# Kernel optimization log

Hardware: AMD Instinct MI355X
Metric: run time of the kernel (lower is better)

## Reference

```python
import jax, jax.numpy as jnp
import numpy as np

H = 4  # head_num = 8 // 2
NEG = -1e9


def mha(x, mask, wqkv, bqkv, wo, bo):
    # x: [B, N, D], mask: [B, 1, N] (0 = masked key), wqkv: [3, D, D], wo: [D, Dout]
    B, N, D = x.shape
    dh = D // H
    q = (x @ wqkv[0] + bqkv[0]).reshape(B, N, H, dh)
    k = (x @ wqkv[1] + bqkv[1]).reshape(B, N, H, dh)
    v = (x @ wqkv[2] + bqkv[2]).reshape(B, N, H, dh)
    scores = jnp.einsum('bqhd,bkhd->bhqk', q, k) / jnp.sqrt(jnp.asarray(dh, x.dtype))
    scores = jnp.where(mask[:, None, :, :] == 0, NEG, scores)  # mask keys, bcast over heads/queries
    attn = jax.nn.softmax(scores, axis=-1)
    out = jnp.einsum('bhqk,bkhd->bqhd', attn, v).reshape(B, N, D)
    return out @ wo + bo


def setup_inputs() -> dict:
    key = jax.random.key(0)
    ks = jax.random.split(key, 24)
    B, M, F = 16, 32, 16
    N = M * M
    def w(k, shape, fan_in):
        return jax.random.normal(k, shape, dtype=jnp.float32) / np.sqrt(fan_in)
    return {
        'robot_1_node': jax.random.normal(ks[0], (B, M, F), dtype=jnp.float32),
        'robot_2_node': jax.random.normal(ks[1], (B, M, F), dtype=jnp.float32),
        'coop_edge_cost': jax.random.normal(ks[2], (B, M, M, F), dtype=jnp.float32),
        'coop_edge_mask': jax.random.randint(ks[3], (B, M, M), 0, 2, dtype=jnp.int32),
        'd1_wqkv': w(ks[4], (3, 48, 48), 48), 'd1_bqkv': jnp.zeros((3, 48), jnp.float32),
        'd1_wo': w(ks[5], (48, 16), 48), 'd1_bo': jnp.zeros((16,), jnp.float32),
        'd2_wqkv': w(ks[6], (3, 16, 16), 16), 'd2_bqkv': jnp.zeros((3, 16), jnp.float32),
        'd2_wo': w(ks[7], (16, 16), 16), 'd2_bo': jnp.zeros((16,), jnp.float32),
        'pol_wqkv': w(ks[8], (3, 16, 16), 16), 'pol_bqkv': jnp.zeros((3, 16), jnp.float32),
        'pol_wo': w(ks[9], (16, 1), 16), 'pol_bo': jnp.zeros((1,), jnp.float32),
        'val_wqkv': w(ks[10], (3, 16, 16), 16), 'val_bqkv': jnp.zeros((3, 16), jnp.float32),
        'val_wo': w(ks[11], (16, 1), 16), 'val_bo': jnp.zeros((1,), jnp.float32),
        'v2_w': w(ks[12], (N, 16), N), 'v2_b': jnp.zeros((16,), jnp.float32),
    }


def reference(robot_1_node, robot_2_node, coop_edge_cost, coop_edge_mask,
              d1_wqkv, d1_bqkv, d1_wo, d1_bo,
              d2_wqkv, d2_bqkv, d2_wo, d2_bo,
              pol_wqkv, pol_bqkv, pol_wo, pol_bo,
              val_wqkv, val_bqkv, val_wo, val_bo,
              v2_w, v2_b):
    B, M, F = robot_1_node.shape
    N = M * M
    edge = coop_edge_cost.reshape(B, N, -1)            # flatten(-3,-2)
    mask = coop_edge_mask.reshape(B, 1, N)             # flatten + unsqueeze(-2)
    f1 = jnp.broadcast_to(robot_1_node[:, :, None, :], (B, M, M, F)).reshape(B, N, F)
    f2 = jnp.broadcast_to(robot_2_node[:, None, :, :], (B, M, M, F)).reshape(B, N, F)
    f = jnp.concatenate([f1, f2, edge], axis=-1)       # [B, N, 3F]
    e = mha(f, mask, d1_wqkv, d1_bqkv, d1_wo, d1_bo)   # [B, N, 16]
    e = mha(e, mask, d2_wqkv, d2_bqkv, d2_wo, d2_bo)   # [B, N, 16]
    action = mha(e, mask, pol_wqkv, pol_bqkv, pol_wo, pol_bo).reshape(B, N)
    masked_action = jax.nn.softmax(jnp.where(mask[:, 0, :] == 0, NEG, action), axis=-1)
    critic = mha(e, mask, val_wqkv, val_bqkv, val_wo, val_bo).reshape(B, N)
    critic = critic @ v2_w + v2_b                       # [B, 16]
    return masked_action, critic
```

## Files before the change

kernel.cpp:

```cpp
#include <hip/hip_runtime.h>
#include <math.h>

#define NEGV (-1e9f)
#define LOG2E 1.4426950408889634f

typedef _Float16 f16;
typedef __attribute__((ext_vector_type(2))) __fp16 hf2;
typedef __attribute__((ext_vector_type(4))) _Float16 f16x4;
typedef __attribute__((ext_vector_type(4))) float f32x4;

__global__ void qkv1_prep_kernel(
    const float* __restrict__ r1, const float* __restrict__ r2,
    const float* __restrict__ edge,
    const float* __restrict__ d1_wqkv, const float* __restrict__ d1_bqkv,
    const float* __restrict__ d1_wo, const float* __restrict__ d1_bo,
    const float* __restrict__ d2_wqkv, const float* __restrict__ d2_bqkv,
    const float* __restrict__ d2_wo, const float* __restrict__ d2_bo,
    const float* __restrict__ pol_wqkv, const float* __restrict__ pol_bqkv,
    const float* __restrict__ val_wqkv, const float* __restrict__ val_bqkv,
    f16* __restrict__ q1h, f16* __restrict__ k1h, f16* __restrict__ v1h,
    float* __restrict__ Wf1, float* __restrict__ bf1,
    float* __restrict__ Wfp, float* __restrict__ bfp,
    float* __restrict__ Wfv, float* __restrict__ bfv,
    int B, int M, int F, int H, float qmul1, int mainBlocks) {
    const int N = M * M;
    const int BN = B * N;

    if ((int)blockIdx.x < mainBlocks) {
        int t = blockIdx.x * blockDim.x + threadIdx.x;
        if (t >= 3 * BN * 48) return;
        int col = t % 48;
        int row = (t / 48) % BN;
        int mat = t / (48 * BN);
        int b = row / N, n = row % N;
        int i = n / M, j = n % M;

        const float* f1 = r1 + (b * M + i) * F;
        const float* f2 = r2 + (b * M + j) * F;
        const float* fe = edge + (size_t)row * F;
        const float* w  = d1_wqkv + mat * 48 * 48 + col;

        float s = d1_bqkv[mat * 48 + col];
#pragma unroll
        for (int d = 0; d < 16; ++d) s = fmaf(f1[d], w[d * 48], s);
#pragma unroll
        for (int d = 0; d < 16; ++d) s = fmaf(f2[d], w[(16 + d) * 48], s);
#pragma unroll
        for (int d = 0; d < 16; ++d) s = fmaf(fe[d], w[(32 + d) * 48], s);

        int h = col / 12, dd = col % 12;
        size_t off = ((size_t)(b * H + h) * N + n) * 12 + dd;
        if (mat == 0)      q1h[off] = (f16)(s * qmul1);
        else if (mat == 1) k1h[off] = (f16)s;
        else               v1h[off] = (f16)s;
        return;
    }

    int t = (blockIdx.x - mainBlocks) * blockDim.x + threadIdx.x;
    if (t < 2304) {
        int mat = t / 768, r = (t % 768) / 16, c = t % 16;
        float s = 0.f;
#pragma unroll
        for (int k = 0; k < 16; ++k)
            s = fmaf(d1_wo[r * 16 + k], d2_wqkv[mat * 256 + k * 16 + c], s);
        Wf1[t] = s;
        return;
    }
    int u = t - 2304;
    if (u < 48) {
        int mat = u / 16, c = u % 16;
        float s = d2_bqkv[mat * 16 + c];
#pragma unroll
        for (int k = 0; k < 16; ++k)
            s = fmaf(d1_bo[k], d2_wqkv[mat * 256 + k * 16 + c], s);
        bf1[u] = s;
        return;
    }
    u -= 48;
    if (u < 768) {
        int mat = u / 256, r = (u % 256) / 16, c = u % 16;
        float s = 0.f;
#pragma unroll
        for (int k = 0; k < 16; ++k)
            s = fmaf(d2_wo[r * 16 + k], pol_wqkv[mat * 256 + k * 16 + c], s);
        Wfp[u] = s;
        return;
    }
    u -= 768;
    if (u < 48) {
        int mat = u / 16, c = u % 16;
        float s = pol_bqkv[mat * 16 + c];
#pragma unroll
        for (int k = 0; k < 16; ++k)
            s = fmaf(d2_bo[k], pol_wqkv[mat * 256 + k * 16 + c], s);
        bfp[u] = s;
        return;
    }
    u -= 48;
    if (u < 768) {
        int mat = u / 256, r = (u % 256) / 16, c = u % 16;
        float s = 0.f;
#pragma unroll
        for (int k = 0; k < 16; ++k)
            s = fmaf(d2_wo[r * 16 + k], val_wqkv[mat * 256 + k * 16 + c], s);
        Wfv[u] = s;
        return;
    }
    u -= 768;
    if (u < 48) {
        int mat = u / 16, c = u % 16;
        float s = val_bqkv[mat * 16 + c];
#pragma unroll
        for (int k = 0; k < 16; ++k)
            s = fmaf(d2_bo[k], val_wqkv[mat * 256 + k * 16 + c], s);
        bfv[u] = s;
    }
}

template <int DH, int QT>
__global__ __launch_bounds__(256, 8) void attn_h_kernel(
    const f16* __restrict__ qh1, const f16* __restrict__ kh1, const f16* __restrict__ vh1,
    const f16* __restrict__ qh2, const f16* __restrict__ kh2, const f16* __restrict__ vh2,
    const int* __restrict__ mask,
    float* __restrict__ pacc1, float* __restrict__ pl1,
    float* __restrict__ pacc2, float* __restrict__ pl2,
    int B, int H, int N) {
    const int LD = H * DH;
    const int BH = B * H;

    int bhs = blockIdx.x;
    const f16* qh; const f16* kh; const f16* vh;
    float* pacc; float* pl;
    if (bhs < BH) { qh = qh1; kh = kh1; vh = vh1; pacc = pacc1; pl = pl1; }
    else          { qh = qh2; kh = kh2; vh = vh2; pacc = pacc2; pl = pl2; bhs -= BH; }
    int b = bhs / H, h = bhs % H;
    int kbase = blockIdx.z * 256;
    int bN = b * N;

    __shared__ __align__(16) f16 Kt[256][DH];
    __shared__ __align__(16) f16 Vt[16][264];
    __shared__ __align__(16) float mbs[256];

    int tid = threadIdx.x;
    {
        int kk = tid;
        const f16* kB = kh + ((size_t)bhs * N + kbase) * DH;
        const f16* vB = vh + ((size_t)bhs * N + kbase) * DH;
#pragma unroll
        for (int d = 0; d < DH / 4; ++d)
            ((uint2*)&Kt[kk][0])[d] = ((const uint2*)(kB + (size_t)kk * DH))[d];
        uint2 vr[DH / 4];
#pragma unroll
        for (int d = 0; d < DH / 4; ++d)
            vr[d] = ((const uint2*)(vB + (size_t)kk * DH))[d];
        const f16* vv = (const f16*)vr;
#pragma unroll
        for (int d = 0; d < DH; ++d) Vt[d][kk] = vv[d];
        Vt[DH][kk] = (f16)1.f;
        mbs[kk] = mask[bN + kbase + kk] ? (-8.f * LOG2E) : NEGV;
    }
    __syncthreads();

    int lane = tid & 63, wid = tid >> 6;
    int lrow = lane & 15, lg = lane >> 4;
    int qbase = blockIdx.y * (QT * 64) + wid * (QT * 16);

    const f16* qB = qh + (size_t)bhs * N * DH;
    f16x4 zf = {(f16)0.f, (f16)0.f, (f16)0.f, (f16)0.f};
    bool qok = (4 * lg < DH);
    f16x4 qf[QT];
#pragma unroll
    for (int qt = 0; qt < QT; ++qt)
        qf[qt] = qok ? *(const f16x4*)(qB + (size_t)(qbase + qt * 16 + lrow) * DH + 4 * lg) : zf;

    f32x4 oacc[QT];
#pragma unroll
    for (int qt = 0; qt < QT; ++qt) oacc[qt] = (f32x4){0.f, 0.f, 0.f, 0.f};

#pragma unroll 8
    for (int t16 = 0; t16 < 16; ++t16) {
        f16x4 kf = *(const f16x4*)(&Kt[0][0] + (size_t)(t16 * 16 + lrow) * DH + 4 * lg);
        float4 mv = *(const float4*)(&mbs[t16 * 16 + 4 * lg]);
        f32x4 mc = {mv.x, mv.y, mv.z, mv.w};
        f16x4 vb = *(const f16x4*)(&Vt[lrow][t16 * 16 + 4 * lg]);

#pragma unroll
        for (int qt = 0; qt < QT; ++qt) {
            f32x4 s = __builtin_amdgcn_mfma_f32_16x16x16f16(kf, qf[qt], mc, 0, 0, 0);
            hf2 lo = __builtin_amdgcn_cvt_pkrtz(__builtin_amdgcn_exp2f(s[0]),
                                                __builtin_amdgcn_exp2f(s[1]));
            hf2 hi = __builtin_amdgcn_cvt_pkrtz(__builtin_amdgcn_exp2f(s[2]),
                                                __builtin_amdgcn_exp2f(s[3]));
            f16x4 pa;
            ((hf2*)&pa)[0] = lo;
            ((hf2*)&pa)[1] = hi;
            oacc[qt] = __builtin_amdgcn_mfma_f32_16x16x16f16(pa, vb, oacc[qt], 0, 0, 0);
        }
    }

    int d = lrow;
    size_t zoff = (size_t)blockIdx.z * B * N;
#pragma unroll
    for (int qt = 0; qt < QT; ++qt) {
#pragma unroll
        for (int r = 0; r < 4; ++r) {
            int q = qbase + qt * 16 + lg * 4 + r;
            float val = oacc[qt][r];
            if (d < DH)
                pacc[(zoff + bN + q) * LD + h * DH + d] = val;
            else if (d == DH)
                pl[(zoff + bN + q) * H + h] = val;
        }
    }
}

__global__ __launch_bounds__(256) void fold1_kernel(
    const float* __restrict__ pacc, const float* __restrict__ pl,
    const float* __restrict__ Wf1, const float* __restrict__ bf1,
    f16* __restrict__ q2h, f16* __restrict__ k2h, f16* __restrict__ v2h,
    int BN, int N, int H, float qmul2) {
    int row0 = blockIdx.x * 16;
    int tid = threadIdx.x;
    __shared__ float comb[16][49];
    __shared__ float invl[16][4];
    if (tid < 64) {
        int r = tid >> 2, h = tid & 3;
        float ls = 0.f;
#pragma unroll
        for (int z = 0; z < 4; ++z) ls += pl[((size_t)z * BN + row0 + r) * 4 + h];
        invl[r][h] = 1.f / ls;
    }
    __syncthreads();
#pragma unroll
    for (int k = 0; k < 3; ++k) {
        int idx = tid + k * 256;
        int r = idx / 48, d = idx % 48;
        float a = 0.f;
#pragma unroll
        for (int z = 0; z < 4; ++z) a += pacc[((size_t)z * BN + row0 + r) * 48 + d];
        comb[r][d] = a * invl[r][d / 12];
    }
    __syncthreads();
#pragma unroll
    for (int k = 0; k < 3; ++k) {
        int idx = tid + k * 256;
        int mat = idx / 256, r = (idx % 256) / 16, c = idx % 16;
        float s = bf1[mat * 16 + c];
        const float* wcol = Wf1 + mat * 768 + c;
#pragma unroll
        for (int d = 0; d < 48; ++d)
            s = fmaf(comb[r][d], wcol[d * 16], s);
        int row = row0 + r;
        int b = row / N, n = row % N;
        int h = c >> 2, dd = c & 3;
        size_t off = ((size_t)(b * H + h) * N + n) * 4 + dd;
        if (mat == 0)      q2h[off] = (f16)(s * qmul2);
        else if (mat == 1) k2h[off] = (f16)s;
        else               v2h[off] = (f16)s;
    }
}

__global__ __launch_bounds__(256) void fold2_kernel(
    const float* __restrict__ pacc, const float* __restrict__ pl,
    const float* __restrict__ Wfp, const float* __restrict__ bfp,
    const float* __restrict__ Wfv, const float* __restrict__ bfv,
    f16* __restrict__ qph, f16* __restrict__ kph, f16* __restrict__ vph,
    f16* __restrict__ qvh, f16* __restrict__ kvh, f16* __restrict__ vvh,
    int BN, int N, int H, float qmul2) {
    int row0 = blockIdx.x * 8;
    int tid = threadIdx.x;
    __shared__ float comb[8][17];
    __shared__ float invl[8][4];
    if (tid < 32) {
        int r = tid >> 2, h = tid & 3;
        float ls = 0.f;
#pragma unroll
        for (int z = 0; z < 4; ++z) ls += pl[((size_t)z * BN + row0 + r) * 4 + h];
        invl[r][h] = 1.f / ls;
    }
    __syncthreads();
    if (tid < 128) {
        int r = tid / 16, d = tid % 16;
        float a = 0.f;
#pragma unroll
        for (int z = 0; z < 4; ++z) a += pacc[((size_t)z * BN + row0 + r) * 16 + d];
        comb[r][d] = a * invl[r][d >> 2];
    }
    __syncthreads();
#pragma unroll
    for (int k = 0; k < 3; ++k) {
        int idx = tid + k * 256;
        int set = idx / 384;
        int rem = idx % 384;
        int mat = rem / 128, r = (rem % 128) / 16, c = rem % 16;
        const float* W  = set ? Wfv : Wfp;
        const float* bb = set ? bfv : bfp;
        float s = bb[mat * 16 + c];
        const float* wcol = W + mat * 256 + c;
#pragma unroll
        for (int d = 0; d < 16; ++d)
            s = fmaf(comb[r][d], wcol[d * 16], s);
        int row = row0 + r;
        int b = row / N, n = row % N;
        int h = c >> 2, dd = c & 3;
        size_t off = ((size_t)(b * H + h) * N + n) * 4 + dd;
        f16* dst;
        if (set == 0) dst = (mat == 0) ? qph : (mat == 1) ? kph : vph;
        else          dst = (mat == 0) ? qvh : (mat == 1) ? kvh : vvh;
        dst[off] = (f16)((mat == 0) ? s * qmul2 : s);
    }
}

__global__ __launch_bounds__(256) void final2_kernel(
    const float* __restrict__ paccp, const float* __restrict__ plp,
    const float* __restrict__ paccv, const float* __restrict__ plv,
    const float* __restrict__ pol_wo, const float* __restrict__ pol_bo,
    const float* __restrict__ val_wo, const float* __restrict__ val_bo,
    const int* __restrict__ mask, const float* __restrict__ v2w,
    const float* __restrict__ v2b,
    float* __restrict__ out_action, float* __restrict__ out_critic,
    int N, int B, int BN) {
    int tid = threadIdx.x;
    if ((int)blockIdx.x < B) {
        int b = blockIdx.x;
        int lane = tid & 63, wid = tid >> 6;
        __shared__ float wred[4];
        __shared__ float sbcast;

        float local[4];
        float mx = -INFINITY;
#pragma unroll
        for (int i = 0; i < 4; ++i) {
            int row = b * N + tid + i * 256;
            float sa = pol_bo[0];
            float ls0 = 0.f, ls1 = 0.f, ls2 = 0.f, ls3 = 0.f;
#pragma unroll
            for (int z = 0; z < 4; ++z) {
                const float* plr = plp + ((size_t)z * BN + row) * 4;
                ls0 += plr[0]; ls1 += plr[1]; ls2 += plr[2]; ls3 += plr[3];
            }
            float inv[4] = {1.f / ls0, 1.f / ls1, 1.f / ls2, 1.f / ls3};
#pragma unroll
            for (int d = 0; d < 16; ++d) {
                float a = 0.f;
#pragma unroll
                for (int z = 0; z < 4; ++z)
                    a += paccp[((size_t)z * BN + row) * 16 + d];
                sa = fmaf(a * inv[d >> 2], pol_wo[d], sa);
            }
            float aa = (mask[row] == 0) ? NEGV : sa;
            local[i] = aa;
            mx = fmaxf(mx, aa);
        }
#pragma unroll
        for (int o = 32; o > 0; o >>= 1) mx = fmaxf(mx, __shfl_down(mx, o));
        if (lane == 0) wred[wid] = mx;
        __syncthreads();
        if (tid == 0) sbcast = fmaxf(fmaxf(wred[0], wred[1]), fmaxf(wred[2], wred[3]));
        __syncthreads();
        mx = sbcast;

        float s = 0.f;
#pragma unroll
        for (int i = 0; i < 4; ++i) {
            float p = __expf(local[i] - mx);
            local[i] = p;
            s += p;
        }
#pragma unroll
        for (int o = 32; o > 0; o >>= 1) s += __shfl_down(s, o);
        if (lane == 0) wred[wid] = s;
        __syncthreads();
        if (tid == 0) sbcast = wred[0] + wred[1] + wred[2] + wred[3];
        __syncthreads();
        float inv = 1.f / sbcast;
#pragma unroll
        for (int i = 0; i < 4; ++i) out_action[b * N + tid + i * 256] = local[i] * inv;
    } else {
        int b = blockIdx.x - B;
        __shared__ float cr[1024];
        __shared__ float red[16][17];
#pragma unroll
        for (int i = 0; i < 4; ++i) {
            int idx = tid + i * 256;
            int row = b * N + idx;
            float sc = val_bo[0];
            float ls0 = 0.f, ls1 = 0.f, ls2 = 0.f, ls3 = 0.f;
#pragma unroll
            for (int z = 0; z < 4; ++z) {
                const float* plr = plv + ((size_t)z * BN + row) * 4;
                ls0 += plr[0]; ls1 += plr[1]; ls2 += plr[2]; ls3 += plr[3];
            }
            float inv[4] = {1.f / ls0, 1.f / ls1, 1.f / ls2, 1.f / ls3};
#pragma unroll
            for (int d = 0; d < 16; ++d) {
                float a = 0.f;
#pragma unroll
                for (int z = 0; z < 4; ++z)
                    a += paccv[((size_t)z * BN + row) * 16 + d];
                sc = fmaf(a * inv[d >> 2], val_wo[d], sc);
            }
            cr[idx] = sc;
        }
        __syncthreads();
        int c = tid & 15, seg = tid >> 4;
        float s = 0.f;
        int n0 = seg * 64;
        for (int n = n0; n < n0 + 64; ++n)
            s = fmaf(cr[n], v2w[n * 16 + c], s);
        red[seg][c] = s;
        __syncthreads();
        if (tid < 16) {
            float acc = v2b[tid];
#pragma unroll
            for (int g = 0; g < 16; ++g) acc += red[g][tid];
            out_critic[b * 16 + tid] = acc;
        }
    }
}

extern "C" void kernel_launch(void* const* d_in, const int* in_sizes, int n_in,
                              void* d_out, int out_size, void* d_ws, size_t ws_size,
                              hipStream_t stream) {
    const int B = 16, M = 32, F = 16, H = 4;
    const int N = M * M;
    const int BN = B * N;
    const int BHN = B * H * N;
    const int KSPLIT = 4;

    const float* r1       = (const float*)d_in[0];
    const float* r2       = (const float*)d_in[1];
    const float* edge     = (const float*)d_in[2];
    const int*   mask     = (const int*)d_in[3];
    const float* d1_wqkv  = (const float*)d_in[4];
    const float* d1_bqkv  = (const float*)d_in[5];
    const float* d1_wo    = (const float*)d_in[6];
    const float* d1_bo    = (const float*)d_in[7];
    const float* d2_wqkv  = (const float*)d_in[8];
    const float* d2_bqkv  = (const float*)d_in[9];
    const float* d2_wo    = (const float*)d_in[10];
    const float* d2_bo    = (const float*)d_in[11];
    const float* pol_wqkv = (const float*)d_in[12];
    const float* pol_bqkv = (const float*)d_in[13];
    const float* pol_wo   = (const float*)d_in[14];
    const float* pol_bo   = (const float*)d_in[15];
    const float* val_wqkv = (const float*)d_in[16];
    const float* val_bqkv = (const float*)d_in[17];
    const float* val_wo   = (const float*)d_in[18];
    const float* val_bo   = (const float*)d_in[19];
    const float* v2_w     = (const float*)d_in[20];
    const float* v2_b     = (const float*)d_in[21];

    float* ws = (float*)d_ws;
    float* pacc = ws;
    float* plp  = pacc + 4 * BN * 48;
    float* plv  = plp + 4 * BN * 4;
    float* Wf1  = plv + 4 * BN * 4;
    float* bf1  = Wf1 + 2304;
    float* Wfp  = bf1 + 48;
    float* bfp  = Wfp + 768;
    float* Wfv  = bfp + 48;
    float* bfv  = Wfv + 768;
    f16* fh  = (f16*)(bfv + 48);
    f16* q1h = fh;
    f16* k1h = q1h + (size_t)BHN * 12;
    f16* v1h = k1h + (size_t)BHN * 12;
    f16* q2h = v1h + (size_t)BHN * 12;
    f16* k2h = q2h + (size_t)BHN * 4;
    f16* v2h = k2h + (size_t)BHN * 4;
    f16* qph = v2h + (size_t)BHN * 4;
    f16* kph = qph + (size_t)BHN * 4;
    f16* vph = kph + (size_t)BHN * 4;
    f16* qvh = vph + (size_t)BHN * 4;
    f16* kvh = qvh + (size_t)BHN * 4;
    f16* vvh = kvh + (size_t)BHN * 4;
    float* paccp = pacc;
    float* paccv = pacc + (size_t)KSPLIT * BN * 16;

    float* out_action = (float*)d_out;
    float* out_critic = out_action + BN;

    const float qmul1 = (1.0f / sqrtf(12.0f)) * LOG2E;
    const float qmul2 = 0.5f * LOG2E;

    {
        int mainBlocks = (3 * BN * 48 + 255) / 256;
        qkv1_prep_kernel<<<mainBlocks + 16, 256, 0, stream>>>(
            r1, r2, edge, d1_wqkv, d1_bqkv, d1_wo, d1_bo,
            d2_wqkv, d2_bqkv, d2_wo, d2_bo,
            pol_wqkv, pol_bqkv, val_wqkv, val_bqkv,
            q1h, k1h, v1h, Wf1, bf1, Wfp, bfp, Wfv, bfv,
            B, M, F, H, qmul1, mainBlocks);
    }
    attn_h_kernel<12, 2><<<dim3(B * H, N / 128, KSPLIT), 256, 0, stream>>>(
        q1h, k1h, v1h, q1h, k1h, v1h, mask,
        pacc, plp, pacc, plp, B, H, N);
    fold1_kernel<<<BN / 16, 256, 0, stream>>>(
        pacc, plp, Wf1, bf1, q2h, k2h, v2h, BN, N, H, qmul2);
    attn_h_kernel<4, 2><<<dim3(B * H, N / 128, KSPLIT), 256, 0, stream>>>(
        q2h, k2h, v2h, q2h, k2h, v2h, mask,
        pacc, plp, pacc, plp, B, H, N);
    fold2_kernel<<<BN / 8, 256, 0, stream>>>(
        pacc, plp, Wfp, bfp, Wfv, bfv,
        qph, kph, vph, qvh, kvh, vvh, BN, N, H, qmul2);
    attn_h_kernel<4, 2><<<dim3(2 * B * H, N / 128, KSPLIT), 256, 0, stream>>>(
        qph, kph, vph, qvh, kvh, vvh, mask,
        paccp, plp, paccv, plv, B, H, N);
    final2_kernel<<<2 * B, 256, 0, stream>>>(
        paccp, plp, paccv, plv, pol_wo, pol_bo, val_wo, val_bo,
        mask, v2_w, v2_b, out_action, out_critic, N, B, BN);
}
```

Baseline: 105.0 us.

## Fuse attention with fold projections and drop split-K partial buffers

Each attention layer is restructured so one 512-thread block handles 32 queries across all 4 heads of one batch. It loops over all 1024 keys in four shared-memory chunks instead of splitting keys over grid z and writing partial accumulators. The normalized per-head output stays in shared memory and goes straight into the next layer's QKV projection (or the pol/val output head), which removes the separate fold kernels and the partial-sum global round trips. The cost is less grid parallelism, a longer serial key loop per block, and extra barriers per chunk.

```diff
diff --git a/kernel.cpp b/kernel.cpp
--- a/kernel.cpp
+++ b/kernel.cpp
@@ -56,7 +56,7 @@
         return;
     }
 
-    int t = (blockIdx.x - mainBlocks) * blockDim.x + threadIdx.x;
+    int t = (blockIdx.x - mainBlocks) * 256 + threadIdx.x;
     if (t < 2304) {
         int mat = t / 768, r = (t % 768) / 16, c = t % 16;
         float s = 0.f;
@@ -117,76 +117,58 @@
     }
 }
 
-template <int DH, int QT>
-__global__ __launch_bounds__(256, 8) void attn_h_kernel(
-    const f16* __restrict__ qh1, const f16* __restrict__ kh1, const f16* __restrict__ vh1,
-    const f16* __restrict__ qh2, const f16* __restrict__ kh2, const f16* __restrict__ vh2,
-    const int* __restrict__ mask,
-    float* __restrict__ pacc1, float* __restrict__ pl1,
-    float* __restrict__ pacc2, float* __restrict__ pl2,
-    int B, int H, int N) {
-    const int LD = H * DH;
-    const int BH = B * H;
-
-    int bhs = blockIdx.x;
-    const f16* qh; const f16* kh; const f16* vh;
-    float* pacc; float* pl;
-    if (bhs < BH) { qh = qh1; kh = kh1; vh = vh1; pacc = pacc1; pl = pl1; }
-    else          { qh = qh2; kh = kh2; vh = vh2; pacc = pacc2; pl = pl2; bhs -= BH; }
-    int b = bhs / H, h = bhs % H;
-    int kbase = blockIdx.z * 256;
-    int bN = b * N;
-
-    __shared__ __align__(16) f16 Kt[256][DH];
-    __shared__ __align__(16) f16 Vt[16][264];
-    __shared__ __align__(16) float mbs[256];
-
+template <int DH>
+__device__ inline void attn_core(const f16* __restrict__ qh, const f16* __restrict__ kh,
+                                 const f16* __restrict__ vh, const int* __restrict__ mask,
+                                 int b, int qg, int H, int N,
+                                 f16* __restrict__ Kt, f16* __restrict__ Vt,
+                                 float* __restrict__ mbs,
+                                 float* __restrict__ comb, int combStride) {
     int tid = threadIdx.x;
-    {
-        int kk = tid;
-        const f16* kB = kh + ((size_t)bhs * N + kbase) * DH;
-        const f16* vB = vh + ((size_t)bhs * N + kbase) * DH;
-#pragma unroll
-        for (int d = 0; d < DH / 4; ++d)
-            ((uint2*)&Kt[kk][0])[d] = ((const uint2*)(kB + (size_t)kk * DH))[d];
-        uint2 vr[DH / 4];
-#pragma unroll
-        for (int d = 0; d < DH / 4; ++d)
-            vr[d] = ((const uint2*)(vB + (size_t)kk * DH))[d];
-        const f16* vv = (const f16*)vr;
-#pragma unroll
-        for (int d = 0; d < DH; ++d) Vt[d][kk] = vv[d];
-        Vt[DH][kk] = (f16)1.f;
-        mbs[kk] = mask[bN + kbase + kk] ? (-8.f * LOG2E) : NEGV;
-    }
-    __syncthreads();
-
-    int lane = tid & 63, wid = tid >> 6;
+    int wave = tid >> 6, lane = tid & 63;
+    int h = wave & 3, qhalf = wave >> 2;
     int lrow = lane & 15, lg = lane >> 4;
-    int qbase = blockIdx.y * (QT * 64) + wid * (QT * 16);
-
-    const f16* qB = qh + (size_t)bhs * N * DH;
+    int bhs = b * H + h;
+    int qrow = qg * 32 + qhalf * 16 + lrow;
+
     f16x4 zf = {(f16)0.f, (f16)0.f, (f16)0.f, (f16)0.f};
     bool qok = (4 * lg < DH);
-    f16x4 qf[QT];
-#pragma unroll
-    for (int qt = 0; qt < QT; ++qt)
-        qf[qt] = qok ? *(const f16x4*)(qB + (size_t)(qbase + qt * 16 + lrow) * DH + 4 * lg) : zf;
-
-    f32x4 oacc[QT];
-#pragma unroll
-    for (int qt = 0; qt < QT; ++qt) oacc[qt] = (f32x4){0.f, 0.f, 0.f, 0.f};
-
+    f16x4 qf = qok ? *(const f16x4*)(qh + ((size_t)bhs * N + qrow) * DH + 4 * lg) : zf;
+
+    f32x4 oacc = {0.f, 0.f, 0.f, 0.f};
+
+    for (int chunk = 0; chunk < 4; ++chunk) {
+        int kbase = chunk * 256;
+        __syncthreads();
+        for (int idx = tid; idx < 1024; idx += 512) {
+            int hh = idx >> 8, kk = idx & 255;
+            const f16* kB = kh + ((size_t)(b * H + hh) * N + kbase + kk) * DH;
+            const f16* vB = vh + ((size_t)(b * H + hh) * N + kbase + kk) * DH;
+#pragma unroll
+            for (int d4 = 0; d4 < DH / 4; ++d4)
+                ((uint2*)(Kt + ((size_t)hh * 256 + kk) * DH))[d4] = ((const uint2*)kB)[d4];
+            uint2 vr[DH / 4];
+#pragma unroll
+            for (int d4 = 0; d4 < DH / 4; ++d4) vr[d4] = ((const uint2*)vB)[d4];
+            const f16* vv = (const f16*)vr;
+#pragma unroll
+            for (int d = 0; d < DH; ++d)
+                Vt[(hh * (DH + 1) + d) * 264 + kk] = vv[d];
+            Vt[(hh * (DH + 1) + DH) * 264 + kk] = (f16)1.f;
+        }
+        if (tid < 256) mbs[tid] = mask[b * N + kbase + tid] ? (-8.f * LOG2E) : NEGV;
+        __syncthreads();
+
+        const f16* KtH = Kt + (size_t)h * 256 * DH;
+        const f16* VtH = Vt + (size_t)h * (DH + 1) * 264;
 #pragma unroll 8
-    for (int t16 = 0; t16 < 16; ++t16) {
-        f16x4 kf = *(const f16x4*)(&Kt[0][0] + (size_t)(t16 * 16 + lrow) * DH + 4 * lg);
-        float4 mv = *(const float4*)(&mbs[t16 * 16 + 4 * lg]);
-        f32x4 mc = {mv.x, mv.y, mv.z, mv.w};
-        f16x4 vb = *(const f16x4*)(&Vt[lrow][t16 * 16 + 4 * lg]);
-
-#pragma unroll
-        for (int qt = 0; qt < QT; ++qt) {
-            f32x4 s = __builtin_amdgcn_mfma_f32_16x16x16f16(kf, qf[qt], mc, 0, 0, 0);
+        for (int t16 = 0; t16 < 16; ++t16) {
+            f16x4 kf = *(const f16x4*)(KtH + (size_t)(t16 * 16 + lrow) * DH + 4 * lg);
+            float4 mv = *(const float4*)(mbs + t16 * 16 + 4 * lg);
+            f32x4 mc = {mv.x, mv.y, mv.z, mv.w};
+            f16x4 vb = *(const f16x4*)(VtH + (size_t)lrow * 264 + t16 * 16 + 4 * lg);
+
+            f32x4 s = __builtin_amdgcn_mfma_f32_16x16x16f16(kf, qf, mc, 0, 0, 0);
             hf2 lo = __builtin_amdgcn_cvt_pkrtz(__builtin_amdgcn_exp2f(s[0]),
                                                 __builtin_amdgcn_exp2f(s[1]));
             hf2 hi = __builtin_amdgcn_cvt_pkrtz(__builtin_amdgcn_exp2f(s[2]),
@@ -194,116 +176,90 @@
             f16x4 pa;
             ((hf2*)&pa)[0] = lo;
             ((hf2*)&pa)[1] = hi;
-            oacc[qt] = __builtin_amdgcn_mfma_f32_16x16x16f16(pa, vb, oacc[qt], 0, 0, 0);
+            oacc = __builtin_amdgcn_mfma_f32_16x16x16f16(pa, vb, oacc, 0, 0, 0);
         }
     }
 
-    int d = lrow;
-    size_t zoff = (size_t)blockIdx.z * B * N;
-#pragma unroll
-    for (int qt = 0; qt < QT; ++qt) {
-#pragma unroll
-        for (int r = 0; r < 4; ++r) {
-            int q = qbase + qt * 16 + lg * 4 + r;
-            float val = oacc[qt][r];
-            if (d < DH)
-                pacc[(zoff + bN + q) * LD + h * DH + d] = val;
-            else if (d == DH)
-                pl[(zoff + bN + q) * H + h] = val;
-        }
-    }
-}
-
-__global__ __launch_bounds__(256) void fold1_kernel(
-    const float* __restrict__ pacc, const float* __restrict__ pl,
+    __syncthreads();
+#pragma unroll
+    for (int r = 0; r < 4; ++r) {
+        float lr = __shfl(oacc[r], (lane & 48) | DH);
+        if (lrow < DH)
+            comb[(qhalf * 16 + lg * 4 + r) * combStride + h * DH + lrow] = oacc[r] / lr;
+    }
+    __syncthreads();
+}
+
+__global__ __launch_bounds__(512, 4) void attn1_fold1_kernel(
+    const f16* __restrict__ q1h, const f16* __restrict__ k1h, const f16* __restrict__ v1h,
+    const int* __restrict__ mask,
     const float* __restrict__ Wf1, const float* __restrict__ bf1,
     f16* __restrict__ q2h, f16* __restrict__ k2h, f16* __restrict__ v2h,
-    int BN, int N, int H, float qmul2) {
-    int row0 = blockIdx.x * 16;
+    int H, int N, float qmul2) {
+    const int DH = 12;
+    const int VROWS = 3 * (DH + 1) + 16;
+    __shared__ __align__(16) f16 KtA[4 * 256 * DH];
+    __shared__ __align__(16) f16 VtA[VROWS * 264];
+    __shared__ __align__(16) float mbsA[256];
+
+    int qg = blockIdx.x, b = blockIdx.y;
+    float* comb = (float*)KtA;
+    attn_core<DH>(q1h, k1h, v1h, mask, b, qg, H, N, KtA, VtA, mbsA, comb, 49);
+
     int tid = threadIdx.x;
-    __shared__ float comb[16][49];
-    __shared__ float invl[16][4];
-    if (tid < 64) {
-        int r = tid >> 2, h = tid & 3;
-        float ls = 0.f;
-#pragma unroll
-        for (int z = 0; z < 4; ++z) ls += pl[((size_t)z * BN + row0 + r) * 4 + h];
-        invl[r][h] = 1.f / ls;
-    }
-    __syncthreads();
 #pragma unroll
     for (int k = 0; k < 3; ++k) {
-        int idx = tid + k * 256;
-        int r = idx / 48, d = idx % 48;
-        float a = 0.f;
-#pragma unroll
-        for (int z = 0; z < 4; ++z) a += pacc[((size_t)z * BN + row0 + r) * 48 + d];
-        comb[r][d] = a * invl[r][d / 12];
-    }
-    __syncthreads();
-#pragma unroll
-    for (int k = 0; k < 3; ++k) {
-        int idx = tid + k * 256;
-        int mat = idx / 256, r = (idx % 256) / 16, c = idx % 16;
+        int idx = tid + k * 512;
+        int mat = idx / 512, r = (idx % 512) / 16, c = idx % 16;
         float s = bf1[mat * 16 + c];
         const float* wcol = Wf1 + mat * 768 + c;
 #pragma unroll
         for (int d = 0; d < 48; ++d)
-            s = fmaf(comb[r][d], wcol[d * 16], s);
-        int row = row0 + r;
-        int b = row / N, n = row % N;
-        int h = c >> 2, dd = c & 3;
-        size_t off = ((size_t)(b * H + h) * N + n) * 4 + dd;
+            s = fmaf(comb[r * 49 + d], wcol[d * 16], s);
+        int n = qg * 32 + r;
+        int hh = c >> 2, dd = c & 3;
+        size_t off = ((size_t)(b * H + hh) * N + n) * 4 + dd;
         if (mat == 0)      q2h[off] = (f16)(s * qmul2);
         else if (mat == 1) k2h[off] = (f16)s;
         else               v2h[off] = (f16)s;
     }
 }
 
-__global__ __launch_bounds__(256) void fold2_kernel(
-    const float* __restrict__ pacc, const float* __restrict__ pl,
+__global__ __launch_bounds__(512, 8) void attn2_fold2_kernel(
+    const f16* __restrict__ q2h, const f16* __restrict__ k2h, const f16* __restrict__ v2h,
+    const int* __restrict__ mask,
     const float* __restrict__ Wfp, const float* __restrict__ bfp,
     const float* __restrict__ Wfv, const float* __restrict__ bfv,
     f16* __restrict__ qph, f16* __restrict__ kph, f16* __restrict__ vph,
     f16* __restrict__ qvh, f16* __restrict__ kvh, f16* __restrict__ vvh,
-    int BN, int N, int H, float qmul2) {
-    int row0 = blockIdx.x * 8;
+    int H, int N, float qmul2) {
+    const int DH = 4;
+    const int VROWS = 3 * (DH + 1) + 16;
+    __shared__ __align__(16) f16 KtA[4 * 256 * DH];
+    __shared__ __align__(16) f16 VtA[VROWS * 264];
+    __shared__ __align__(16) float mbsA[256];
+
+    int qg = blockIdx.x, b = blockIdx.y;
+    float* comb = (float*)KtA;
+    attn_core<DH>(q2h, k2h, v2h, mask, b, qg, H, N, KtA, VtA, mbsA, comb, 17);
+
     int tid = threadIdx.x;
-    __shared__ float comb[8][17];
-    __shared__ float invl[8][4];
-    if (tid < 32) {
-        int r = tid >> 2, h = tid & 3;
-        float ls = 0.f;
-#pragma unroll
-        for (int z = 0; z < 4; ++z) ls += pl[((size_t)z * BN + row0 + r) * 4 + h];
-        invl[r][h] = 1.f / ls;
-    }
-    __syncthreads();
-    if (tid < 128) {
-        int r = tid / 16, d = tid % 16;
-        float a = 0.f;
-#pragma unroll
-        for (int z = 0; z < 4; ++z) a += pacc[((size_t)z * BN + row0 + r) * 16 + d];
-        comb[r][d] = a * invl[r][d >> 2];
-    }
-    __syncthreads();
-#pragma unroll
-    for (int k = 0; k < 3; ++k) {
-        int idx = tid + k * 256;
-        int set = idx / 384;
-        int rem = idx % 384;
-        int mat = rem / 128, r = (rem % 128) / 16, c = rem % 16;
+#pragma unroll
+    for (int k = 0; k < 6; ++k) {
+        int idx = tid + k * 512;
+        int set = idx / 1536;
+        int rem = idx % 1536;
+        int mat = rem / 512, r = (rem % 512) / 16, c = rem % 16;
         const float* W  = set ? Wfv : Wfp;
         const float* bb = set ? bfv : bfp;
         float s = bb[mat * 16 + c];
         const float* wcol = W + mat * 256 + c;
 #pragma unroll
         for (int d = 0; d < 16; ++d)
-            s = fmaf(comb[r][d], wcol[d * 16], s);
-        int row = row0 + r;
-        int b = row / N, n = row % N;
-        int h = c >> 2, dd = c & 3;
-        size_t off = ((size_t)(b * H + h) * N + n) * 4 + dd;
+            s = fmaf(comb[r * 17 + d], wcol[d * 16], s);
+        int n = qg * 32 + r;
+        int hh = c >> 2, dd = c & 3;
+        size_t off = ((size_t)(b * H + hh) * N + n) * 4 + dd;
         f16* dst;
         if (set == 0) dst = (mat == 0) ? qph : (mat == 1) ? kph : vph;
         else          dst = (mat == 0) ? qvh : (mat == 1) ? kvh : vvh;
@@ -311,15 +267,43 @@
     }
 }
 
-__global__ __launch_bounds__(256) void final2_kernel(
-    const float* __restrict__ paccp, const float* __restrict__ plp,
-    const float* __restrict__ paccv, const float* __restrict__ plv,
+__global__ __launch_bounds__(512, 8) void attn3_heads_kernel(
+    const f16* __restrict__ qph, const f16* __restrict__ kph, const f16* __restrict__ vph,
+    const f16* __restrict__ qvh, const f16* __restrict__ kvh, const f16* __restrict__ vvh,
+    const int* __restrict__ mask,
     const float* __restrict__ pol_wo, const float* __restrict__ pol_bo,
     const float* __restrict__ val_wo, const float* __restrict__ val_bo,
-    const int* __restrict__ mask, const float* __restrict__ v2w,
+    float* __restrict__ araw, float* __restrict__ craw,
+    int H, int N) {
+    const int DH = 4;
+    const int VROWS = 3 * (DH + 1) + 16;
+    __shared__ __align__(16) f16 KtA[4 * 256 * DH];
+    __shared__ __align__(16) f16 VtA[VROWS * 264];
+    __shared__ __align__(16) float mbsA[256];
+
+    int qg = blockIdx.x, b = blockIdx.y, set = blockIdx.z;
+    const f16* qh = set ? qvh : qph;
+    const f16* kh = set ? kvh : kph;
+    const f16* vh = set ? vvh : vph;
+    float* comb = (float*)KtA;
+    attn_core<DH>(qh, kh, vh, mask, b, qg, H, N, KtA, VtA, mbsA, comb, 17);
+
+    int tid = threadIdx.x;
+    if (tid < 32) {
+        int r = tid;
+        const float* wo = set ? val_wo : pol_wo;
+        float s = (set ? val_bo : pol_bo)[0];
+#pragma unroll
+        for (int d = 0; d < 16; ++d) s = fmaf(comb[r * 17 + d], wo[d], s);
+        (set ? craw : araw)[b * N + qg * 32 + r] = s;
+    }
+}
+
+__global__ __launch_bounds__(256) void final_kernel(
+    const float* __restrict__ araw, const int* __restrict__ mask,
+    const float* __restrict__ craw, const float* __restrict__ v2w,
     const float* __restrict__ v2b,
-    float* __restrict__ out_action, float* __restrict__ out_critic,
-    int N, int B, int BN) {
+    float* __restrict__ out_action, float* __restrict__ out_critic, int N, int B) {
     int tid = threadIdx.x;
     if ((int)blockIdx.x < B) {
         int b = blockIdx.x;
@@ -331,26 +315,11 @@
         float mx = -INFINITY;
 #pragma unroll
         for (int i = 0; i < 4; ++i) {
-            int row = b * N + tid + i * 256;
-            float sa = pol_bo[0];
-            float ls0 = 0.f, ls1 = 0.f, ls2 = 0.f, ls3 = 0.f;
-#pragma unroll
-            for (int z = 0; z < 4; ++z) {
-                const float* plr = plp + ((size_t)z * BN + row) * 4;
-                ls0 += plr[0]; ls1 += plr[1]; ls2 += plr[2]; ls3 += plr[3];
-            }
-            float inv[4] = {1.f / ls0, 1.f / ls1, 1.f / ls2, 1.f / ls3};
-#pragma unroll
-            for (int d = 0; d < 16; ++d) {
-                float a = 0.f;
-#pragma unroll
-                for (int z = 0; z < 4; ++z)
-                    a += paccp[((size_t)z * BN + row) * 16 + d];
-                sa = fmaf(a * inv[d >> 2], pol_wo[d], sa);
-            }
-            float aa = (mask[row] == 0) ? NEGV : sa;
-            local[i] = aa;
-            mx = fmaxf(mx, aa);
+            int n = tid + i * 256;
+            float a = araw[b * N + n];
+            if (mask[b * N + n] == 0) a = NEGV;
+            local[i] = a;
+            mx = fmaxf(mx, a);
         }
 #pragma unroll
         for (int o = 32; o > 0; o >>= 1) mx = fmaxf(mx, __shfl_down(mx, o));
@@ -378,36 +347,12 @@
         for (int i = 0; i < 4; ++i) out_action[b * N + tid + i * 256] = local[i] * inv;
     } else {
         int b = blockIdx.x - B;
-        __shared__ float cr[1024];
+        int c = tid & 15, seg = tid >> 4;
         __shared__ float red[16][17];
-#pragma unroll
-        for (int i = 0; i < 4; ++i) {
-            int idx = tid + i * 256;
-            int row = b * N + idx;
-            float sc = val_bo[0];
-            float ls0 = 0.f, ls1 = 0.f, ls2 = 0.f, ls3 = 0.f;
-#pragma unroll
-            for (int z = 0; z < 4; ++z) {
-                const float* plr = plv + ((size_t)z * BN + row) * 4;
-                ls0 += plr[0]; ls1 += plr[1]; ls2 += plr[2]; ls3 += plr[3];
-            }
-            float inv[4] = {1.f / ls0, 1.f / ls1, 1.f / ls2, 1.f / ls3};
-#pragma unroll
-            for (int d = 0; d < 16; ++d) {
-                float a = 0.f;
-#pragma unroll
-                for (int z = 0; z < 4; ++z)
-                    a += paccv[((size_t)z * BN + row) * 16 + d];
-                sc = fmaf(a * inv[d >> 2], val_wo[d], sc);
-            }
-            cr[idx] = sc;
-        }
-        __syncthreads();
-        int c = tid & 15, seg = tid >> 4;
         float s = 0.f;
         int n0 = seg * 64;
         for (int n = n0; n < n0 + 64; ++n)
-            s = fmaf(cr[n], v2w[n * 16 + c], s);
+            s = fmaf(craw[b * N + n], v2w[n * 16 + c], s);
         red[seg][c] = s;
         __syncthreads();
         if (tid < 16) {
@@ -426,7 +371,6 @@
     const int N = M * M;
     const int BN = B * N;
     const int BHN = B * H * N;
-    const int KSPLIT = 4;
 
     const float* r1       = (const float*)d_in[0];
     const float* r2       = (const float*)d_in[1];
@@ -452,16 +396,15 @@
     const float* v2_b     = (const float*)d_in[21];
 
     float* ws = (float*)d_ws;
-    float* pacc = ws;
-    float* plp  = pacc + 4 * BN * 48;
-    float* plv  = plp + 4 * BN * 4;
-    float* Wf1  = plv + 4 * BN * 4;
+    float* Wf1  = ws;
     float* bf1  = Wf1 + 2304;
     float* Wfp  = bf1 + 48;
     float* bfp  = Wfp + 768;
     float* Wfv  = bfp + 48;
     float* bfv  = Wfv + 768;
-    f16* fh  = (f16*)(bfv + 48);
+    float* araw = bfv + 48;
+    float* craw = araw + BN;
+    f16* fh  = (f16*)(craw + BN);
     f16* q1h = fh;
     f16* k1h = q1h + (size_t)BHN * 12;
     f16* v1h = k1h + (size_t)BHN * 12;
@@ -474,8 +417,6 @@
     f16* qvh = vph + (size_t)BHN * 4;
     f16* kvh = qvh + (size_t)BHN * 4;
     f16* vvh = kvh + (size_t)BHN * 4;
-    float* paccp = pacc;
-    float* paccv = pacc + (size_t)KSPLIT * BN * 16;
 
     float* out_action = (float*)d_out;
     float* out_critic = out_action + BN;
@@ -492,21 +433,14 @@
             q1h, k1h, v1h, Wf1, bf1, Wfp, bfp, Wfv, bfv,
             B, M, F, H, qmul1, mainBlocks);
     }
-    attn_h_kernel<12, 2><<<dim3(B * H, N / 128, KSPLIT), 256, 0, stream>>>(
-        q1h, k1h, v1h, q1h, k1h, v1h, mask,
-        pacc, plp, pacc, plp, B, H, N);
-    fold1_kernel<<<BN / 16, 256, 0, stream>>>(
-        pacc, plp, Wf1, bf1, q2h, k2h, v2h, BN, N, H, qmul2);
-    attn_h_kernel<4, 2><<<dim3(B * H, N / 128, KSPLIT), 256, 0, stream>>>(
-        q2h, k2h, v2h, q2h, k2h, v2h, mask,
-        pacc, plp, pacc, plp, B, H, N);
-    fold2_kernel<<<BN / 8, 256, 0, stream>>>(
-        pacc, plp, Wfp, bfp, Wfv, bfv,
-        qph, kph, vph, qvh, kvh, vvh, BN, N, H, qmul2);
-    attn_h_kernel<4, 2><<<dim3(2 * B * H, N / 128, KSPLIT), 256, 0, stream>>>(
+    attn1_fold1_kernel<<<dim3(N / 32, B), 512, 0, stream>>>(
+        q1h, k1h, v1h, mask, Wf1, bf1, q2h, k2h, v2h, H, N, qmul2);
+    attn2_fold2_kernel<<<dim3(N / 32, B), 512, 0, stream>>>(
+        q2h, k2h, v2h, mask, Wfp, bfp, Wfv, bfv,
+        qph, kph, vph, qvh, kvh, vvh, H, N, qmul2);
+    attn3_heads_kernel<<<dim3(N / 32, B, 2), 512, 0, stream>>>(
         qph, kph, vph, qvh, kvh, vvh, mask,
-        paccp, plp, paccv, plv, B, H, N);
-    final2_kernel<<<2 * B, 256, 0, stream>>>(
-        paccp, plp, paccv, plv, pol_wo, pol_bo, val_wo, val_bo,
-        mask, v2_w, v2_b, out_action, out_critic, N, B, BN);
-}
+        pol_wo, pol_bo, val_wo, val_bo, araw, craw, H, N);
+    final_kernel<<<2 * B, 256, 0, stream>>>(
+        araw, mask, craw, v2_w, v2_b, out_action, out_critic, N, B);
+}
```

Measured after the change: 107.3 us. 1.02x slower.
